# Optimization experiments

Hardware: AMD Instinct MI355X
Metric: run time of the kernel (lower is better)

Reference implementation:

```python
import jax, jax.numpy as jnp
import numpy as np

B, L, H, C = 2, 512, 128, 25

def setup_inputs() -> dict:
    key = jax.random.key(0)
    k1, k2, k3, k4 = jax.random.split(key, 4)
    x1 = jax.random.normal(k1, (B, L, H), dtype=jnp.float32)
    x2 = jax.random.normal(k2, (B, L, H), dtype=jnp.float32)
    W = jax.random.normal(k3, (C, 4 * H), dtype=jnp.float32) * (1.0 / np.sqrt(4 * H))
    b = jax.random.normal(k4, (C,), dtype=jnp.float32) * 0.01
    return {"x1": x1, "x2": x2, "W": W, "b": b}

def reference(x1, x2, W, b):
    # feat = cat([x1_i, x2_j, x1_i*x2_j, |x1_i - x2_j|]) over all (i, j) pairs,
    # then Linear(4H -> C). Split W into its 4 H-sized blocks so we never
    # materialize the [B, L, L, 4H] concatenated tensor.
    Hd = x1.shape[-1]
    W1, W2, W3, W4 = (W[:, 0:Hd], W[:, Hd:2*Hd], W[:, 2*Hd:3*Hd], W[:, 3*Hd:4*Hd])
    a = x1[:, :, None, :]   # [B, L, 1, H] -> row token
    c = x2[:, None, :, :]   # [B, 1, L, H] -> col token
    # a@W1 and c@W2 depend on only one index, so compute [B, L, C] then broadcast.
    t1 = jnp.einsum('blh,ch->blc', x1, W1)[:, :, None, :]  # [B, L, 1, C]
    t2 = jnp.einsum('blh,ch->blc', x2, W2)[:, None, :, :]  # [B, 1, L, C]
    # product term is a bilinear contraction; no [B,L,L,H] materialization needed.
    t3 = jnp.einsum('blh,bmh,ch->blmc', x1, x2, W3)         # [B, L, L, C]
    # abs-diff term requires the pairwise [B, L, L, H] tensor (nonlinear in pair).
    t4 = jnp.einsum('blmh,ch->blmc', jnp.abs(a - c), W4)    # [B, L, L, C]
    return t1 + t2 + t3 + t4 + b  # [B, L, L, C]
```

## Files before the change

kernel.cpp:

```cpp
#include <hip/hip_runtime.h>
#include <hip/hip_bf16.h>
#include <math.h>

#define BB 2
#define LL 512
#define HH 128
#define CC 25
#define W4H (4*HH)

typedef __attribute__((ext_vector_type(8))) short short8;
typedef __attribute__((ext_vector_type(4))) float f32x4;

#define T1_OFF 0
#define T2_OFF (BB*LL*CC)
#define WFT_BYTE_OFF (2*BB*LL*CC*4)

#define MTILE 64
#define LPB   8
#define XP    132

static __device__ __forceinline__ short f2bf(float f) {
    return __builtin_bit_cast(short, __float2bfloat16(f));
}

__global__ __launch_bounds__(256)
void prep_kernel(const float* __restrict__ x1, const float* __restrict__ x2,
                 const float* __restrict__ W, const float* __restrict__ bias,
                 float* __restrict__ ws)
{
    const int tid = threadIdx.x;
    const int c   = blockIdx.y;
    const int bl  = blockIdx.x * 256 + tid;

    if (blockIdx.y == 0) {
        unsigned short* wft = (unsigned short*)((char*)ws + WFT_BYTE_OFF);
        for (int idx = blockIdx.x * 256 + tid; idx < 32 * 256; idx += 4 * 256) {
            const int cc = idx >> 8;
            const int k  = idx & 255;
            float v = 0.f;
            if (cc < CC) v = (k < HH) ? W[(size_t)cc * W4H + 2*HH + k]
                                      : W[(size_t)cc * W4H + 3*HH + (k - HH)];
            wft[idx] = (unsigned short)f2bf(v);
        }
    }

    const float* w1  = W + (size_t)c * W4H;
    const float* w2  = w1 + HH;
    const float* xr1 = x1 + (size_t)bl * HH;
    const float* xr2 = x2 + (size_t)bl * HH;

    float s1a = 0.f, s1b = 0.f, s2a = 0.f, s2b = 0.f;
    #pragma unroll
    for (int i = 0; i < 32; i += 2) {
        const f32x4 a0 = *(const f32x4*)(xr1 + i*4);
        const f32x4 a1 = *(const f32x4*)(xr1 + i*4 + 4);
        const f32x4 b0 = *(const f32x4*)(xr2 + i*4);
        const f32x4 b1 = *(const f32x4*)(xr2 + i*4 + 4);
        const f32x4 u0 = *(const f32x4*)(w1 + i*4);
        const f32x4 u1 = *(const f32x4*)(w1 + i*4 + 4);
        const f32x4 v0 = *(const f32x4*)(w2 + i*4);
        const f32x4 v1 = *(const f32x4*)(w2 + i*4 + 4);
        #pragma unroll
        for (int j = 0; j < 4; ++j) {
            s1a = fmaf(a0[j], u0[j], s1a);
            s1b = fmaf(a1[j], u1[j], s1b);
            s2a = fmaf(b0[j], v0[j], s2a);
            s2b = fmaf(b1[j], v1[j], s2b);
        }
    }
    ws[T1_OFF + bl * CC + c] = s1a + s1b + bias[c];
    ws[T2_OFF + bl * CC + c] = s2a + s2b;
}

__global__ __launch_bounds__(256)
void biaffine_mfma(const float* __restrict__ x1, const float* __restrict__ x2,
                   const float* __restrict__ ws, float* __restrict__ out)
{
    __shared__ __align__(16) float x2s[MTILE * XP];
    __shared__ __align__(16) float x1s[LPB * HH];

    const int tid = threadIdx.x;
    const int b   = blockIdx.z;
    const int l0  = blockIdx.y * LPB;
    const int m0  = blockIdx.x * MTILE;

    const int lane = tid & 63;
    const int wv   = tid >> 6;
    const int q    = lane >> 4;
    const int cn   = lane & 15;

    const unsigned short* wft = (const unsigned short*)((const char*)ws + WFT_BYTE_OFF);
    short8 Bf[2][8];
    #pragma unroll
    for (int t = 0; t < 2; ++t)
        #pragma unroll
        for (int kk = 0; kk < 8; ++kk)
            Bf[t][kk] = *(const short8*)(wft + ((cn + 16*t) * 256 + kk * 32 + q * 8));

    {
        const float* sx2 = x2 + ((size_t)b * LL + m0) * HH;
        #pragma unroll
        for (int i = 0; i < 8; ++i) {
            const int idx = i * 256 + tid;
            const int r   = idx >> 5;
            const int c4  = idx & 31;
            f32x4 v = *(const f32x4*)(sx2 + r * HH + c4 * 4);
            *(f32x4*)(&x2s[r * XP + c4 * 4]) = v;
        }
        const float* sx1 = x1 + ((size_t)b * LL + l0) * HH;
        f32x4 v = *(const f32x4*)(sx1 + tid * 4);
        *(f32x4*)(&x1s[tid * 4]) = v;
    }
    __syncthreads();

    const int mrowA = wv * 16 + cn;
    const float* px2 = &x2s[mrowA * XP];

    f32x4 acc0[LPB], acc1[LPB];
    #pragma unroll
    for (int l = 0; l < LPB; ++l) {
        acc0[l] = (f32x4){0.f, 0.f, 0.f, 0.f};
        acc1[l] = (f32x4){0.f, 0.f, 0.f, 0.f};
    }

    #pragma unroll
    for (int hh = 0; hh < 4; ++hh) {
        const int hb = hh * 32 + q * 8;
        const f32x4 b0 = *(const f32x4*)(px2 + hb);
        const f32x4 b1 = *(const f32x4*)(px2 + hb + 4);
        #pragma unroll
        for (int l = 0; l < LPB; ++l) {
            const float* px1 = &x1s[l * HH];
            const f32x4 a0 = *(const f32x4*)(px1 + hb);
            const f32x4 a1 = *(const f32x4*)(px1 + hb + 4);
            short8 Ap, Ad;
            #pragma unroll
            for (int j = 0; j < 4; ++j) {
                Ap[j]     = f2bf(a0[j] * b0[j]);
                Ad[j]     = f2bf(fabsf(a0[j] - b0[j]));
                Ap[4 + j] = f2bf(a1[j] * b1[j]);
                Ad[4 + j] = f2bf(fabsf(a1[j] - b1[j]));
            }
            acc0[l] = __builtin_amdgcn_mfma_f32_16x16x32_bf16(Ap, Bf[0][hh],     acc0[l], 0, 0, 0);
            acc1[l] = __builtin_amdgcn_mfma_f32_16x16x32_bf16(Ap, Bf[1][hh],     acc1[l], 0, 0, 0);
            acc0[l] = __builtin_amdgcn_mfma_f32_16x16x32_bf16(Ad, Bf[0][hh + 4], acc0[l], 0, 0, 0);
            acc1[l] = __builtin_amdgcn_mfma_f32_16x16x32_bf16(Ad, Bf[1][hh + 4], acc1[l], 0, 0, 0);
        }
    }

    const float* Tb1 = ws + T1_OFF;
    const float* Tb2 = ws + T2_OFF;

    float t2a[4], t2b[4];
    #pragma unroll
    for (int r = 0; r < 4; ++r) {
        const int mg = m0 + wv * 16 + q * 4 + r;
        t2a[r] = Tb2[((size_t)b * LL + mg) * CC + cn];
        t2b[r] = (cn + 16 < CC) ? Tb2[((size_t)b * LL + mg) * CC + cn + 16] : 0.f;
    }

    #pragma unroll
    for (int l = 0; l < LPB; ++l) {
        const int lg = l0 + l;
        const float t1a = Tb1[((size_t)b * LL + lg) * CC + cn];
        const float t1b = (cn + 16 < CC) ? Tb1[((size_t)b * LL + lg) * CC + cn + 16] : 0.f;
        #pragma unroll
        for (int r = 0; r < 4; ++r) {
            const int mg = m0 + wv * 16 + q * 4 + r;
            float* o = out + (((size_t)b * LL + lg) * LL + mg) * CC;
            o[cn] = acc0[l][r] + t1a + t2a[r];
            if (cn + 16 < CC) o[cn + 16] = acc1[l][r] + t1b + t2b[r];
        }
    }
}

extern "C" void kernel_launch(void* const* d_in, const int* in_sizes, int n_in,
                              void* d_out, int out_size, void* d_ws, size_t ws_size,
                              hipStream_t stream) {
    const float* x1   = (const float*)d_in[0];
    const float* x2   = (const float*)d_in[1];
    const float* W    = (const float*)d_in[2];
    const float* bias = (const float*)d_in[3];
    float* out = (float*)d_out;
    float* ws  = (float*)d_ws;

    dim3 pgrid(BB * LL / 256, CC);
    prep_kernel<<<pgrid, 256, 0, stream>>>(x1, x2, W, bias, ws);

    dim3 grid(LL / MTILE, LL / LPB, BB);
    biaffine_mfma<<<grid, 256, 0, stream>>>(x1, x2, ws, out);
}
```

Baseline: 111.9 us.

## Switch pairwise features to packed fp16 math with f16 MFMA and per-row accumulation

Inputs are converted to fp16 once when staged into shared memory, so the product and abs-diff features are built with packed half-precision vector ops instead of per-element fp32 math followed by bf16 conversion. The weights move to fp16 and the MFMA switches to the f16 variant. The loop is also reordered so each l row accumulates and stores right away, with the x2 fragments held in registers, which shrinks live accumulators. In exchange, fp16 range and precision limits apply to the inputs, products and differences, and round-toward-zero conversion is used.

```diff
diff --git a/kernel.cpp b/kernel.cpp
--- a/kernel.cpp
+++ b/kernel.cpp
@@ -8,8 +8,10 @@
 #define CC 25
 #define W4H (4*HH)
 
-typedef __attribute__((ext_vector_type(8))) short short8;
-typedef __attribute__((ext_vector_type(4))) float f32x4;
+typedef __attribute__((ext_vector_type(4))) float    f32x4;
+typedef __attribute__((ext_vector_type(8))) _Float16 half8;
+typedef __attribute__((ext_vector_type(2))) _Float16 half2t;
+typedef __attribute__((ext_vector_type(4))) unsigned uint4v;
 
 #define T1_OFF 0
 #define T2_OFF (BB*LL*CC)
@@ -17,11 +19,19 @@
 
 #define MTILE 64
 #define LPB   8
-#define XP    132
+#define XPH   136
 
-static __device__ __forceinline__ short f2bf(float f) {
-    return __builtin_bit_cast(short, __float2bfloat16(f));
+static __device__ __forceinline__ half8 habs8(half8 x) {
+    uint4v u = __builtin_bit_cast(uint4v, x);
+    u &= 0x7FFF7FFFu;
+    return __builtin_bit_cast(half8, u);
 }
+
+static __device__ __forceinline__ half2t pkrtz(float a, float b) {
+    return __builtin_bit_cast(half2t, __builtin_amdgcn_cvt_pkrtz(a, b));
+}
+
+union H4 { half2t h2[2]; unsigned long long u64; };
 
 __global__ __launch_bounds__(256)
 void prep_kernel(const float* __restrict__ x1, const float* __restrict__ x2,
@@ -33,14 +43,14 @@
     const int bl  = blockIdx.x * 256 + tid;
 
     if (blockIdx.y == 0) {
-        unsigned short* wft = (unsigned short*)((char*)ws + WFT_BYTE_OFF);
+        _Float16* wft = (_Float16*)((char*)ws + WFT_BYTE_OFF);
         for (int idx = blockIdx.x * 256 + tid; idx < 32 * 256; idx += 4 * 256) {
             const int cc = idx >> 8;
             const int k  = idx & 255;
             float v = 0.f;
             if (cc < CC) v = (k < HH) ? W[(size_t)cc * W4H + 2*HH + k]
                                       : W[(size_t)cc * W4H + 3*HH + (k - HH)];
-            wft[idx] = (unsigned short)f2bf(v);
+            wft[idx] = (_Float16)v;
         }
     }
 
@@ -76,8 +86,8 @@
 void biaffine_mfma(const float* __restrict__ x1, const float* __restrict__ x2,
                    const float* __restrict__ ws, float* __restrict__ out)
 {
-    __shared__ __align__(16) float x2s[MTILE * XP];
-    __shared__ __align__(16) float x1s[LPB * HH];
+    __shared__ __align__(16) _Float16 x2h[MTILE * XPH];
+    __shared__ __align__(16) _Float16 x1h[LPB * XPH];
 
     const int tid = threadIdx.x;
     const int b   = blockIdx.z;
@@ -89,13 +99,13 @@
     const int q    = lane >> 4;
     const int cn   = lane & 15;
 
-    const unsigned short* wft = (const unsigned short*)((const char*)ws + WFT_BYTE_OFF);
-    short8 Bf[2][8];
+    const _Float16* wft = (const _Float16*)((const char*)ws + WFT_BYTE_OFF);
+    half8 Bf[2][8];
     #pragma unroll
     for (int t = 0; t < 2; ++t)
         #pragma unroll
         for (int kk = 0; kk < 8; ++kk)
-            Bf[t][kk] = *(const short8*)(wft + ((cn + 16*t) * 256 + kk * 32 + q * 8));
+            Bf[t][kk] = *(const half8*)(wft + ((cn + 16*t) * 256 + kk * 32 + q * 8));
 
     {
         const float* sx2 = x2 + ((size_t)b * LL + m0) * HH;
@@ -104,53 +114,31 @@
             const int idx = i * 256 + tid;
             const int r   = idx >> 5;
             const int c4  = idx & 31;
-            f32x4 v = *(const f32x4*)(sx2 + r * HH + c4 * 4);
-            *(f32x4*)(&x2s[r * XP + c4 * 4]) = v;
+            const f32x4 v = *(const f32x4*)(sx2 + r * HH + c4 * 4);
+            H4 h;
+            h.h2[0] = pkrtz(v[0], v[1]);
+            h.h2[1] = pkrtz(v[2], v[3]);
+            *(unsigned long long*)(&x2h[r * XPH + c4 * 4]) = h.u64;
         }
         const float* sx1 = x1 + ((size_t)b * LL + l0) * HH;
-        f32x4 v = *(const f32x4*)(sx1 + tid * 4);
-        *(f32x4*)(&x1s[tid * 4]) = v;
+        const int r  = tid >> 5;
+        const int c4 = tid & 31;
+        const f32x4 v = *(const f32x4*)(sx1 + r * HH + c4 * 4);
+        H4 h;
+        h.h2[0] = pkrtz(v[0], v[1]);
+        h.h2[1] = pkrtz(v[2], v[3]);
+        *(unsigned long long*)(&x1h[r * XPH + c4 * 4]) = h.u64;
     }
     __syncthreads();
 
     const int mrowA = wv * 16 + cn;
-    const float* px2 = &x2s[mrowA * XP];
-
-    f32x4 acc0[LPB], acc1[LPB];
+    half8 X2f[4];
     #pragma unroll
-    for (int l = 0; l < LPB; ++l) {
-        acc0[l] = (f32x4){0.f, 0.f, 0.f, 0.f};
-        acc1[l] = (f32x4){0.f, 0.f, 0.f, 0.f};
-    }
-
-    #pragma unroll
-    for (int hh = 0; hh < 4; ++hh) {
-        const int hb = hh * 32 + q * 8;
-        const f32x4 b0 = *(const f32x4*)(px2 + hb);
-        const f32x4 b1 = *(const f32x4*)(px2 + hb + 4);
-        #pragma unroll
-        for (int l = 0; l < LPB; ++l) {
-            const float* px1 = &x1s[l * HH];
-            const f32x4 a0 = *(const f32x4*)(px1 + hb);
-            const f32x4 a1 = *(const f32x4*)(px1 + hb + 4);
-            short8 Ap, Ad;
-            #pragma unroll
-            for (int j = 0; j < 4; ++j) {
-                Ap[j]     = f2bf(a0[j] * b0[j]);
-                Ad[j]     = f2bf(fabsf(a0[j] - b0[j]));
-                Ap[4 + j] = f2bf(a1[j] * b1[j]);
-                Ad[4 + j] = f2bf(fabsf(a1[j] - b1[j]));
-            }
-            acc0[l] = __builtin_amdgcn_mfma_f32_16x16x32_bf16(Ap, Bf[0][hh],     acc0[l], 0, 0, 0);
-            acc1[l] = __builtin_amdgcn_mfma_f32_16x16x32_bf16(Ap, Bf[1][hh],     acc1[l], 0, 0, 0);
-            acc0[l] = __builtin_amdgcn_mfma_f32_16x16x32_bf16(Ad, Bf[0][hh + 4], acc0[l], 0, 0, 0);
-            acc1[l] = __builtin_amdgcn_mfma_f32_16x16x32_bf16(Ad, Bf[1][hh + 4], acc1[l], 0, 0, 0);
-        }
-    }
+    for (int hh = 0; hh < 4; ++hh)
+        X2f[hh] = *(const half8*)(&x2h[mrowA * XPH + hh * 32 + q * 8]);
 
     const float* Tb1 = ws + T1_OFF;
     const float* Tb2 = ws + T2_OFF;
-
     float t2a[4], t2b[4];
     #pragma unroll
     for (int r = 0; r < 4; ++r) {
@@ -164,12 +152,28 @@
         const int lg = l0 + l;
         const float t1a = Tb1[((size_t)b * LL + lg) * CC + cn];
         const float t1b = (cn + 16 < CC) ? Tb1[((size_t)b * LL + lg) * CC + cn + 16] : 0.f;
+
+        f32x4 acc0 = {0.f, 0.f, 0.f, 0.f};
+        f32x4 acc1 = {0.f, 0.f, 0.f, 0.f};
+
+        #pragma unroll
+        for (int hh = 0; hh < 4; ++hh) {
+            const half8 a  = *(const half8*)(&x1h[l * XPH + hh * 32 + q * 8]);
+            const half8 bq = X2f[hh];
+            const half8 Ap = a * bq;
+            const half8 Ad = habs8(a - bq);
+            acc0 = __builtin_amdgcn_mfma_f32_16x16x32_f16(Ap, Bf[0][hh],     acc0, 0, 0, 0);
+            acc1 = __builtin_amdgcn_mfma_f32_16x16x32_f16(Ap, Bf[1][hh],     acc1, 0, 0, 0);
+            acc0 = __builtin_amdgcn_mfma_f32_16x16x32_f16(Ad, Bf[0][hh + 4], acc0, 0, 0, 0);
+            acc1 = __builtin_amdgcn_mfma_f32_16x16x32_f16(Ad, Bf[1][hh + 4], acc1, 0, 0, 0);
+        }
+
         #pragma unroll
         for (int r = 0; r < 4; ++r) {
             const int mg = m0 + wv * 16 + q * 4 + r;
             float* o = out + (((size_t)b * LL + lg) * LL + mg) * CC;
-            o[cn] = acc0[l][r] + t1a + t2a[r];
-            if (cn + 16 < CC) o[cn + 16] = acc1[l][r] + t1b + t2b[r];
+            o[cn] = acc0[r] + t1a + t2a[r];
+            if (cn + 16 < CC) o[cn + 16] = acc1[r] + t1b + t2b[r];
         }
     }
 }
```

Result: faster. 102.2 us (-8.7%).
